# Kernel tuning notes

Measured on AMD Instinct MI355X. Metric: run time of the kernel, lower is better.

## Reference

```python
import jax, jax.numpy as jnp
import numpy as np


def _ln(x, g, b, eps=1e-5):
    m = jnp.mean(x, axis=-1, keepdims=True)
    v = jnp.var(x, axis=-1, keepdims=True)
    return (x - m) * jax.lax.rsqrt(v + eps) * g + b


def setup_inputs() -> dict:
    key = jax.random.key(0)
    ks = jax.random.split(key, 24)
    B, Cin, Cout, Rout, N1, N2 = 8, 256, 512, 256, 4096, 1024
    s = 0.02
    f32 = jnp.float32
    return {
        "l1": jax.random.normal(ks[0], (B, Cin, N1), f32),
        "xyz1": jax.random.normal(ks[1], (B, 3, N1), f32),
        "l2": jax.random.normal(ks[2], (B, Cout, N2), f32),
        "xyz2": jax.random.normal(ks[3], (B, 3, N2), f32),
        # im_choose 1x1 convs (no bias)
        "q1_w": jax.random.normal(ks[4], (Cout, Cin), f32) * s,
        "k1_w": jax.random.normal(ks[5], (Cout, Cin), f32) * s,
        # mlp: Linear(Cin,Cin) -> LN(Cin) -> ReLU -> Linear(Cin,Cout)
        "mlp_w1": jax.random.normal(ks[6], (Cin, Cin), f32) * s,
        "mlp_b1": jnp.zeros((Cin,), f32),
        "mlp_g1": jnp.ones((Cin,), f32),
        "mlp_be1": jnp.zeros((Cin,), f32),
        "mlp_w2": jax.random.normal(ks[7], (Cout, Cin), f32) * s,
        "mlp_b2": jnp.zeros((Cout,), f32),
        # slefAttention 1x1 convs (no bias); pos1 conv is unused in forward
        "qw": jax.random.normal(ks[8], (Cout, Cout), f32) * s,
        "kw": jax.random.normal(ks[9], (Cout, Cout), f32) * s,
        "vw": jax.random.normal(ks[10], (Cout, Cout), f32) * s,
        "posw": jax.random.normal(ks[11], (Cout, 3), f32) * s,
        # IMFF.norm LayerNorm(Cout)
        "norm_g": jnp.ones((Cout,), f32),
        "norm_b": jnp.zeros((Cout,), f32),
        # mlp1: Linear(Cout,Cout) -> LN(Cout) -> ReLU -> Linear(Cout,Rout)
        "m1_w1": jax.random.normal(ks[12], (Cout, Cout), f32) * s,
        "m1_b1": jnp.zeros((Cout,), f32),
        "m1_g": jnp.ones((Cout,), f32),
        "m1_be": jnp.zeros((Cout,), f32),
        "m1_w2": jax.random.normal(ks[13], (Rout, Cout), f32) * s,
        "m1_b2": jnp.zeros((Rout,), f32),
    }


def reference(l1, xyz1, l2, xyz2, q1_w, k1_w, mlp_w1, mlp_b1, mlp_g1, mlp_be1,
              mlp_w2, mlp_b2, qw, kw, vw, posw, norm_g, norm_b,
              m1_w1, m1_b1, m1_g, m1_be, m1_w2, m1_b2):
    Cout = q1_w.shape[0]
    top_k = l2.shape[2]
    scale = jnp.sqrt(jnp.float32(Cout))

    # ---- im_choose: top-k selection of source points via attention row 0 ----
    q1 = jnp.einsum('oc,bcn->bon', q1_w, l1)          # [B,Cout,N1]
    k1 = jnp.einsum('oc,bcn->bon', k1_w, l1)          # [B,Cout,N1]
    e1 = jnp.einsum('bcn,bcm->bnm', q1, k1) / scale   # [B,N1,N1]
    att1 = jax.nn.softmax(e1, axis=-1)
    att_se = att1[:, 0, :]                            # [B,N1]
    _, idx = jax.lax.top_k(att_se, top_k)             # [B,K]
    l1_sel = jnp.take_along_axis(l1, idx[:, None, :], axis=-1)    # [B,Cin,K]
    p1_sel = jnp.take_along_axis(xyz1, idx[:, None, :], axis=-1)  # [B,3,K]

    # ---- mlp on gathered features ----
    h = jnp.swapaxes(l1_sel, 1, 2)                    # [B,K,Cin]
    h = jax.nn.relu(_ln(h @ mlp_w1.T + mlp_b1, mlp_g1, mlp_be1))
    h = h @ mlp_w2.T + mlp_b2                         # [B,K,Cout]
    x2 = jnp.swapaxes(h, 1, 2)                        # [B,Cout,K]

    # ---- slefAttention (cross): x1=l2/xyz2 queries, x2/p1_sel keys+values ----
    pos_q = jnp.einsum('oc,bcn->bon', posw, xyz2)     # [B,Cout,N2]
    pos_k = jnp.einsum('oc,bcn->bon', posw, p1_sel)   # [B,Cout,K]
    q = jnp.einsum('oc,bcn->bon', qw, l2 + pos_q)
    k = jnp.einsum('oc,bcn->bon', kw, x2 + pos_k)
    v = jnp.einsum('oc,bcn->bon', vw, x2)
    e = jnp.einsum('bcn,bcm->bnm', q, k) / scale      # [B,N2,K]
    att = jax.nn.softmax(e, axis=-1)
    o = jnp.einsum('bnm,bcm->bcn', att, v) + l2       # [B,Cout,N2]
    o = jnp.swapaxes(o, 1, 2)                         # [B,N2,Cout]

    # ---- norm + leaky_relu + mlp1 head ----
    o = jax.nn.leaky_relu(_ln(o, norm_g, norm_b), 0.01)
    o = jax.nn.relu(_ln(o @ m1_w1.T + m1_b1, m1_g, m1_be))
    o = o @ m1_w2.T + m1_b2                           # [B,N2,Rout]
    return jnp.swapaxes(o, 1, 2)                      # [B,Rout,N2]
```

## Files before the change

### kernel.cpp

```cpp
#include <hip/hip_runtime.h>
#include <math.h>


typedef __attribute__((ext_vector_type(8))) short short8x;
typedef __attribute__((ext_vector_type(4))) float f32x4;

__device__ __forceinline__ unsigned short f2b(float f) {
  unsigned int u = __float_as_uint(f);
  unsigned int r = u + 0x7FFFu + ((u >> 16) & 1u);
  return (unsigned short)(r >> 16);
}
__device__ __forceinline__ float b2f(unsigned short h) {
  return __uint_as_float(((unsigned int)h) << 16);
}

__device__ __forceinline__ void cp16(const unsigned short* g, unsigned short* l) {
  __builtin_amdgcn_global_load_lds(
      (const __attribute__((address_space(1))) void*)g,
      (__attribute__((address_space(3))) void*)l, 16, 0, 0);
}

__global__ void __launch_bounds__(256) prep_kernel(
    const float* w0, const float* w1, const float* w2, const float* w3,
    const float* w4, const float* w5, const float* w6,
    unsigned short* d0, unsigned short* d1, unsigned short* d2,
    unsigned short* d3, unsigned short* d4, unsigned short* d5,
    unsigned short* d6,
    const float* __restrict__ l1, const float* __restrict__ q1w,
    float* __restrict__ q1v,
    const float* __restrict__ l2, const float* __restrict__ xyz2,
    const float* __restrict__ posw, unsigned short* __restrict__ qinT,
    float* __restrict__ l2T) {
  __shared__ float tile[64][65];
  __shared__ float sx[3][64];
  __shared__ float col[256];
  const int t = threadIdx.x;
  const int y = blockIdx.y;

  if (y == 7) {
    if (blockIdx.x >= 1024) return;
    const int b = blockIdx.x >> 7;
    const int rem = blockIdx.x & 127;
    const int n0 = (rem & 15) * 64, c0 = (rem >> 4) * 64;
    const int tx = t & 63, ty = t >> 6;
    const float* l2b = l2 + (long)b * 512 * 1024;
    for (int r = 0; r < 16; ++r) {
      const int c = ty * 16 + r;
      tile[c][tx] = l2b[(long)(c0 + c) * 1024 + n0 + tx];
    }
    if (ty < 3) sx[ty][tx] = xyz2[((long)b * 3 + ty) * 1024 + n0 + tx];
    __syncthreads();
    const int c = c0 + tx;
    const float p0 = posw[c * 3], p1 = posw[c * 3 + 1], p2 = posw[c * 3 + 2];
    for (int r = 0; r < 16; ++r) {
      const int nl = ty * 16 + r;
      const float val = tile[tx][nl];
      const long o = ((long)b * 1024 + n0 + nl) * 512 + c;
      l2T[o] = val;
      qinT[o] = f2b(val + p0 * sx[0][nl] + p1 * sx[1][nl] + p2 * sx[2][nl]);
    }
    return;
  }
  if (y == 8) {
    if (blockIdx.x >= 64) return;
    const int b = blockIdx.x >> 3;
    const int chunk = blockIdx.x & 7;
    col[t] = l1[(long)b * 256 * 4096 + (long)t * 4096];
    __syncthreads();
    const int lane = t & 63, wid = t >> 6;
    const float4 cv = *(const float4*)&col[lane * 4];
    const int obase = chunk * 64 + wid * 16;
#pragma unroll
    for (int oo = 0; oo < 16; ++oo) {
      const int o = obase + oo;
      const float4 wv = ((const float4*)(q1w + (long)o * 256))[lane];
      float s = wv.x * cv.x + wv.y * cv.y + wv.z * cv.z + wv.w * cv.w;
      s += __shfl_xor(s, 1); s += __shfl_xor(s, 2); s += __shfl_xor(s, 4);
      s += __shfl_xor(s, 8); s += __shfl_xor(s, 16); s += __shfl_xor(s, 32);
      if (lane == 0) q1v[b * 512 + o] = s;
    }
    return;
  }
  const float* src;
  unsigned short* dst;
  int n;
  switch (y) {
    case 0: src = w0; dst = d0; n = 65536; break;
    case 1: src = w1; dst = d1; n = 131072; break;
    case 2: src = w2; dst = d2; n = 262144; break;
    case 3: src = w3; dst = d3; n = 262144; break;
    case 4: src = w4; dst = d4; n = 262144; break;
    case 5: src = w5; dst = d5; n = 262144; break;
    default: src = w6; dst = d6; n = 131072; break;
  }
  const int i = (blockIdx.x * 256 + t) * 4;
  if (i < n) {
    const float4 v = *(const float4*)(src + i);
    ushort4 o;
    o.x = f2b(v.x); o.y = f2b(v.y); o.z = f2b(v.z); o.w = f2b(v.w);
    *(ushort4*)(dst + i) = o;
  }
}

__global__ void __launch_bounds__(256) selB_kernel(
    const float* __restrict__ k1w, const float* __restrict__ q1v,
    float* __restrict__ wvec) {
  const int b = blockIdx.x;
  const int chunk = blockIdx.y;
  __shared__ float qs[64];
  const int t = threadIdx.x;
  if (t < 64) qs[t] = q1v[b * 512 + chunk * 64 + t];
  __syncthreads();
  float s = 0.f;
  const float* kp = k1w + (long)(chunk * 64) * 256 + t;
#pragma unroll 8
  for (int oo = 0; oo < 64; ++oo) s += kp[(long)oo * 256] * qs[oo];
  atomicAdd(&wvec[b * 256 + t], s);
}

__global__ void __launch_bounds__(256) sel_scores_kernel(
    const float* __restrict__ l1, const float* __restrict__ wvec,
    float* __restrict__ scores) {
  const int b = blockIdx.y;
  const int m = blockIdx.x * 256 + threadIdx.x;
  __shared__ float w[256];
  w[threadIdx.x] = wvec[b * 256 + threadIdx.x];
  __syncthreads();
  const float* base = l1 + (long)b * 256 * 4096 + m;
  float s = 0.f;
  for (int c = 0; c < 256; ++c) s += w[c] * base[(long)c * 4096];
  scores[b * 4096 + m] = s;
}

__global__ void __launch_bounds__(256) topk_select_kernel(
    const float* __restrict__ scores, int* __restrict__ idx_out) {
  const int b = blockIdx.x;
  const int t = threadIdx.x;
  __shared__ unsigned int keys[4096];
  __shared__ unsigned int hist[256];
  __shared__ unsigned int sc_prefix, sc_krem;
  __shared__ int s_bin;
  __shared__ unsigned int partial_gt[256], partial_eq[256];

  for (int m = t; m < 4096; m += 256) {
    unsigned int u = __float_as_uint(scores[b * 4096 + m]);
    u ^= (u & 0x80000000u) ? 0xFFFFFFFFu : 0x80000000u;
    keys[m] = u;
  }
  if (t == 0) { sc_prefix = 0u; sc_krem = 1024u; }
  __syncthreads();

  unsigned int prefmask = 0u;
  for (int shift = 24; shift >= 0; shift -= 8) {
    hist[t] = 0u;
    if (t == 0) s_bin = 0;
    __syncthreads();
    const unsigned int prefix = sc_prefix;
    for (int m = t; m < 4096; m += 256) {
      unsigned int key = keys[m];
      if ((key & prefmask) == prefix) atomicAdd(&hist[(key >> shift) & 255u], 1u);
    }
    __syncthreads();
    for (int off = 1; off < 256; off <<= 1) {
      unsigned int v = hist[t] + ((t + off < 256) ? hist[t + off] : 0u);
      __syncthreads();
      hist[t] = v;
      __syncthreads();
    }
    const unsigned int krem = sc_krem;
    if (hist[t] >= krem) atomicMax(&s_bin, t);
    __syncthreads();
    if (t == 0) {
      const int bin = s_bin;
      sc_krem = krem - ((bin < 255) ? hist[bin + 1] : 0u);
      sc_prefix = prefix | ((unsigned int)bin << shift);
    }
    prefmask |= (0xFFu << shift);
    __syncthreads();
  }
  const unsigned int cutoff = sc_prefix;
  const unsigned int need = sc_krem;

  unsigned int gt = 0u, eq = 0u;
  const int base = t * 16;
  for (int i = 0; i < 16; ++i) {
    unsigned int key = keys[base + i];
    gt += (key > cutoff);
    eq += (key == cutoff);
  }
  partial_gt[t] = gt;
  partial_eq[t] = eq;
  __syncthreads();
  for (int off = 1; off < 256; off <<= 1) {
    unsigned int g = partial_gt[t] + ((t >= off) ? partial_gt[t - off] : 0u);
    unsigned int e2 = partial_eq[t] + ((t >= off) ? partial_eq[t - off] : 0u);
    __syncthreads();
    partial_gt[t] = g;
    partial_eq[t] = e2;
    __syncthreads();
  }
  const unsigned int pref_gt = partial_gt[t] - gt;
  const unsigned int pref_eq = partial_eq[t] - eq;
  unsigned int pos = pref_gt + ((pref_eq < need) ? pref_eq : need);
  unsigned int eqr = pref_eq;
  for (int i = 0; i < 16; ++i) {
    unsigned int key = keys[base + i];
    bool sel = (key > cutoff);
    if (key == cutoff) sel = sel || (eqr++ < need);
    if (sel) idx_out[b * 1024 + (pos++)] = base + i;
  }
}

__global__ void __launch_bounds__(256) gather_sel_kernel(
    const float* __restrict__ l1, const float* __restrict__ xyz1,
    const int* __restrict__ idx, unsigned short* __restrict__ l1selT,
    float* __restrict__ p1selT) {
  const int b = blockIdx.z;
  const int j = blockIdx.x * 64 + (threadIdx.x & 63);
  const int cz = blockIdx.y;
  const int cg = threadIdx.x >> 6;
  const int ix = idx[b * 1024 + j];
  const float* src = l1 + (long)b * 256 * 4096 + ix;
  unsigned short* dst = l1selT + ((long)b * 1024 + j) * 256;
#pragma unroll
  for (int it = 0; it < 8; ++it) {
    const int c = cz * 128 + it * 16 + cg * 4;
    const float x0 = src[(long)(c + 0) * 4096];
    const float x1 = src[(long)(c + 1) * 4096];
    const float x2 = src[(long)(c + 2) * 4096];
    const float x3 = src[(long)(c + 3) * 4096];
    ushort4 o;
    o.x = f2b(x0); o.y = f2b(x1); o.z = f2b(x2); o.w = f2b(x3);
    *(ushort4*)&dst[c] = o;
  }
  if (cz == 0 && cg == 0) {
    float* dp = p1selT + ((long)b * 1024 + j) * 3;
#pragma unroll
    for (int d = 0; d < 3; ++d) dp[d] = xyz1[((long)b * 3 + d) * 4096 + ix];
  }
}

template <int BN, int TRA, int TRB, bool BCOL, bool BROW, bool RES, int EPI>
__global__ void __launch_bounds__(256) gemm_u(
    const unsigned short* __restrict__ A, long sA, int ldA,
    const unsigned short* __restrict__ Bt, long sB, int ldB, long sB8,
    void* __restrict__ Yv, long sY, int ldY,
    const float* __restrict__ bias,
    const float* __restrict__ res, long sR,
    int K, float alpha,
    const float* __restrict__ ts1, const float* __restrict__ ts2,
    const float* __restrict__ tg, const float* __restrict__ tb, float tslope,
    float* __restrict__ os1, float* __restrict__ os2,
    const float* __restrict__ kpos, const float* __restrict__ kpw,
    unsigned short* __restrict__ Y2) {
  constexpr int JN = BN / 32;
  __shared__ __align__(16) unsigned short ldsA[2][128 * 32];
  __shared__ __align__(16) unsigned short ldsB[2][BN * 32];
  const int tid = threadIdx.x;
  const int lane = tid & 63;
  const int wv = tid >> 6;
  const int wm = wv >> 1, wn = wv & 1;
  const int n0 = blockIdx.x * BN, m0 = blockIdx.y * 128, b = blockIdx.z;
  A += (long)b * sA;
  Bt += (long)(b & 7) * sB + (long)(b >> 3) * sB8;
  const int lane15 = lane & 15, q = lane >> 4;

  const int srow0 = wv * 32 + (lane >> 2);
  const int srow1 = srow0 + 16;
  const int ks0 = ((lane & 3) ^ ((srow0 >> 1) & 3)) << 3;
  const int ks1 = ((lane & 3) ^ ((srow1 >> 1) & 3)) << 3;
  const unsigned short* gA0 = A + (long)(m0 + srow0) * ldA + ks0;
  const unsigned short* gA1 = A + (long)(m0 + srow1) * ldA + ks1;
  unsigned short* lA0[2] = {&ldsA[0][(wv * 32) * 32], &ldsA[1][(wv * 32) * 32]};
  unsigned short* lA1[2] = {&ldsA[0][(wv * 32 + 16) * 32], &ldsA[1][(wv * 32 + 16) * 32]};
  const int srowB = (BN == 128) ? srow0 : (wv * 16 + (lane >> 2));
  const int ksB = ((lane & 3) ^ ((srowB >> 1) & 3)) << 3;
  const unsigned short* gB0 = Bt + (long)(n0 + srowB) * ldB + ksB;
  const unsigned short* gB1 = Bt + (long)(n0 + srow1) * ldB + ks1;
  unsigned short* lB0[2] = {&ldsB[0][((BN == 128 ? wv * 32 : wv * 16)) * 32],
                            &ldsB[1][((BN == 128 ? wv * 32 : wv * 16)) * 32]};
  unsigned short* lB1[2] = {&ldsB[0][((wv * 32 + 16) * 32) % (BN * 32)],
                            &ldsB[1][((wv * 32 + 16) * 32) % (BN * 32)]};

  constexpr bool TR = (TRA + TRB) != 0;
  constexpr int TROWS = TRA ? 128 : BN;
  constexpr int TSH = (TROWS == 128) ? 7 : 6;
  constexpr int TCH = (TROWS == 128) ? 2 : 1;
  const int trow = tid & (TROWS - 1), tpart = tid >> TSH;
  float t_mu = 0.f, t_rs = 0.f;
  const unsigned short* tsrc = nullptr;
  int toff[2] = {0, 0};
  int tkof = 0;
  if constexpr (TR) {
    const int row0 = (TRA ? m0 : n0) + trow;
    const int ridx = (b & 7) * 1024 + row0;
    const float Cf = (float)K;
    const float s1v = ts1[ridx], s2v = ts2[ridx];
    t_mu = s1v / Cf;
    t_rs = rsqrtf(s2v / Cf - t_mu * t_mu + 1e-5f);
    tkof = tpart * (TCH * 8);
    tsrc = (TRA ? A + (long)row0 * ldA : Bt + (long)row0 * ldB) + tkof;
    const int sw = (trow >> 1) & 3;
#pragma unroll
    for (int c = 0; c < TCH; ++c)
      toff[c] = trow * 32 + (((tpart * TCH + c) ^ sw) << 3);
  }

  auto t_apply = [&](int kk, short8x r0, short8x r1, int buf) {
    unsigned short* base = TRA ? &ldsA[buf][0] : &ldsB[buf][0];
    const short8x rr[2] = {r0, r1};
#pragma unroll
    for (int c = 0; c < TCH; ++c) {
      union { short8x v; unsigned short u[8]; } a0, w0;
      a0.v = rr[c];
      const float4* gp = (const float4*)(tg + kk + tkof + c * 8);
      const float4* bp = (const float4*)(tb + kk + tkof + c * 8);
      const float4 g0 = gp[0], g1 = gp[1];
      const float4 e0 = bp[0], e1 = bp[1];
      const float gg[8] = {g0.x, g0.y, g0.z, g0.w, g1.x, g1.y, g1.z, g1.w};
      const float ee[8] = {e0.x, e0.y, e0.z, e0.w, e1.x, e1.y, e1.z, e1.w};
#pragma unroll
      for (int u = 0; u < 8; ++u) {
        float y = (b2f(a0.u[u]) - t_mu) * t_rs * gg[u] + ee[u];
        y = y > 0.f ? y : tslope * y;
        w0.u[u] = f2b(y);
      }
      *(short8x*)&base[toff[c]] = w0.v;
    }
  };

  short8x tr0 = {}, tr1 = {};
  if constexpr (TR) {
    tr0 = *(const short8x*)(tsrc + 0);
    if constexpr (TCH == 2) tr1 = *(const short8x*)(tsrc + 8);
  }
  if constexpr (!TRA) { cp16(gA0, lA0[0]); cp16(gA1, lA1[0]); }
  if constexpr (!TRB) {
    cp16(gB0, lB0[0]);
    if constexpr (BN == 128) cp16(gB1, lB1[0]);
  }
  if constexpr (TR) t_apply(0, tr0, tr1, 0);

  f32x4 acc[4][JN] = {};
  int cur = 0;
  for (int k0 = 0; k0 < K; k0 += 32) {
    __syncthreads();
    const bool nxt = (k0 + 32 < K);
    if (nxt) {
      const int nk = k0 + 32;
      if constexpr (!TRA) { cp16(gA0 + nk, lA0[cur ^ 1]); cp16(gA1 + nk, lA1[cur ^ 1]); }
      if constexpr (!TRB) {
        cp16(gB0 + nk, lB0[cur ^ 1]);
        if constexpr (BN == 128) cp16(gB1 + nk, lB1[cur ^ 1]);
      }
      if constexpr (TR) {
        tr0 = *(const short8x*)(tsrc + nk);
        if constexpr (TCH == 2) tr1 = *(const short8x*)(tsrc + nk + 8);
      }
    }
    short8x af[4], bfr[JN];
#pragma unroll
    for (int i = 0; i < 4; ++i) {
      const int m = wm * 64 + i * 16 + lane15;
      af[i] = *(const short8x*)&ldsA[cur][m * 32 + ((q ^ ((m >> 1) & 3)) << 3)];
    }
#pragma unroll
    for (int j = 0; j < JN; ++j) {
      const int n = wn * (BN / 2) + j * 16 + lane15;
      bfr[j] = *(const short8x*)&ldsB[cur][n * 32 + ((q ^ ((n >> 1) & 3)) << 3)];
    }
#pragma unroll
    for (int i = 0; i < 4; ++i)
#pragma unroll
      for (int j = 0; j < JN; ++j)
        acc[i][j] = __builtin_amdgcn_mfma_f32_16x16x32_bf16(af[i], bfr[j], acc[i][j], 0, 0, 0);
    if (nxt) {
      if constexpr (TR) t_apply(k0 + 32, tr0, tr1, cur ^ 1);
    }
    cur ^= 1;
  }

  float* Yf = (float*)Yv;
  unsigned short* Yh = (unsigned short*)Yv;
  if constexpr (EPI == 0) Yf += (long)b * sY; else Yh += (long)b * sY;
  if constexpr (EPI == 5) Y2 += (long)b * sY;
  if constexpr (RES) res += (long)b * sR;
  float inv_[4];
  float kq0[4], kq1[4], kq2[4];
  float ssum[4][4], ssq[4][4];
#pragma unroll
  for (int i = 0; i < 4; ++i)
#pragma unroll
    for (int r = 0; r < 4; ++r) { ssum[i][r] = 0.f; ssq[i][r] = 0.f; }

#pragma unroll
  for (int i = 0; i < 4; ++i) {
    if constexpr (EPI == 4) {
#pragma unroll
      for (int r = 0; r < 4; ++r)
        inv_[r] = 1.f / ts1[(b & 7) * 1024 + m0 + wm * 64 + i * 16 + q * 4 + r];
    }
    if constexpr (EPI == 5) {
#pragma unroll
      for (int r = 0; r < 4; ++r) {
        const int m_g = m0 + wm * 64 + i * 16 + q * 4 + r;
        const float* pp = kpos + ((long)b * 1024 + m_g) * 3;
        kq0[r] = pp[0]; kq1[r] = pp[1]; kq2[r] = pp[2];
      }
    }
#pragma unroll
    for (int j = 0; j < JN; ++j) {
      const int n_g = n0 + wn * (BN / 2) + j * 16 + lane15;
      const float bc = BCOL ? bias[n_g] : 0.f;
      float pw0 = 0.f, pw1 = 0.f, pw2 = 0.f;
      if constexpr (EPI == 5) {
        pw0 = kpw[n_g * 3]; pw1 = kpw[n_g * 3 + 1]; pw2 = kpw[n_g * 3 + 2];
      }
#pragma unroll
      for (int r = 0; r < 4; ++r) {
        const int m_g = m0 + wm * 64 + i * 16 + q * 4 + r;
        float y = acc[i][j][r] * alpha;
        if constexpr (EPI == 4) y *= inv_[r];
        if constexpr (BCOL) y += bc;
        if constexpr (BROW) y += bias[m_g];
        if constexpr (RES) y += res[(long)m_g * ldY + n_g];
        if constexpr (EPI == 3) y = __expf(y);
        const long off = (long)m_g * ldY + n_g;
        if constexpr (EPI == 0) Yf[off] = y;
        else Yh[off] = f2b(y);
        if constexpr (EPI == 5)
          Y2[off] = f2b(y + pw0 * kq0[r] + pw1 * kq1[r] + pw2 * kq2[r]);
        if constexpr (EPI == 2 || EPI == 3 || EPI == 4) {
          ssum[i][r] += y; ssq[i][r] += y * y;
        }
      }
    }
  }
  if constexpr (EPI == 2 || EPI == 4) {
#pragma unroll
    for (int i = 0; i < 4; ++i)
#pragma unroll
      for (int r = 0; r < 4; ++r) {
        float s = ssum[i][r], q2 = ssq[i][r];
        s += __shfl_xor(s, 1); q2 += __shfl_xor(q2, 1);
        s += __shfl_xor(s, 2); q2 += __shfl_xor(q2, 2);
        s += __shfl_xor(s, 4); q2 += __shfl_xor(q2, 4);
        s += __shfl_xor(s, 8); q2 += __shfl_xor(q2, 8);
        if (lane15 == 0) {
          const int ridx = (b & 7) * 1024 + m0 + wm * 64 + i * 16 + q * 4 + r;
          atomicAdd(&os1[ridx], s);
          atomicAdd(&os2[ridx], q2);
        }
      }
  } else if constexpr (EPI == 3) {
#pragma unroll
    for (int i = 0; i < 4; ++i)
#pragma unroll
      for (int r = 0; r < 4; ++r) {
        float s = ssum[i][r];
        s += __shfl_xor(s, 1);
        s += __shfl_xor(s, 2);
        s += __shfl_xor(s, 4);
        s += __shfl_xor(s, 8);
        if (lane15 == 0) {
          const int ridx = (b & 7) * 1024 + m0 + wm * 64 + i * 16 + q * 4 + r;
          atomicAdd(&os1[ridx], s);
        }
      }
  }
}

extern "C" void kernel_launch(void* const* d_in, const int* in_sizes, int n_in,
                              void* d_out, int out_size, void* d_ws,
                              size_t ws_size, hipStream_t stream) {
  const float* l1 = (const float*)d_in[0];
  const float* xyz1 = (const float*)d_in[1];
  const float* l2 = (const float*)d_in[2];
  const float* xyz2 = (const float*)d_in[3];
  const float* q1w = (const float*)d_in[4];
  const float* k1w = (const float*)d_in[5];
  const float* mlp_w1 = (const float*)d_in[6];
  const float* mlp_b1 = (const float*)d_in[7];
  const float* mlp_g1 = (const float*)d_in[8];
  const float* mlp_be1 = (const float*)d_in[9];
  const float* mlp_w2 = (const float*)d_in[10];
  const float* mlp_b2 = (const float*)d_in[11];
  const float* qw = (const float*)d_in[12];
  const float* kw = (const float*)d_in[13];
  const float* vw = (const float*)d_in[14];
  const float* posw = (const float*)d_in[15];
  const float* norm_g = (const float*)d_in[16];
  const float* norm_b = (const float*)d_in[17];
  const float* m1_w1 = (const float*)d_in[18];
  const float* m1_b1 = (const float*)d_in[19];
  const float* m1_g = (const float*)d_in[20];
  const float* m1_be = (const float*)d_in[21];
  const float* m1_w2 = (const float*)d_in[22];
  const float* m1_b2 = (const float*)d_in[23];

  char* ws = (char*)d_ws;
  const long MiB = 1048576;
  unsigned short* wb_mlp_w1 = (unsigned short*)(ws + 0);
  unsigned short* wb_mlp_w2 = (unsigned short*)(ws + 131072);
  unsigned short* wb_qw = (unsigned short*)(ws + 393216);
  unsigned short* wb_kw = (unsigned short*)(ws + 917504);
  unsigned short* wb_vw = (unsigned short*)(ws + 1441792);
  unsigned short* wb_m1w1 = (unsigned short*)(ws + 1966080);
  unsigned short* wb_m1w2 = (unsigned short*)(ws + 2490368);
  float* scores = (float*)(ws + 2752512);
  int* idxb = (int*)(ws + 2891776);
  float* p1selT = (float*)(ws + 2924544);
  float* q1v = (float*)(ws + 3022848);
  float* wvec = (float*)(ws + 3399680);
  float* rowsum = (float*)(ws + 3407872);
  float* h1_s1 = (float*)(ws + 3440640);
  float* h1_s2 = (float*)(ws + 3473408);
  float* o_s1 = (float*)(ws + 3506176);
  float* o_s2 = (float*)(ws + 3538944);
  float* g1_s1 = (float*)(ws + 3571712);
  float* g1_s2 = (float*)(ws + 3604480);
  unsigned short* l1selT = (unsigned short*)(ws + 4 * MiB);
  unsigned short* h1 = (unsigned short*)(ws + 8 * MiB);
  unsigned short* x2T = (unsigned short*)(ws + 12 * MiB);
  unsigned short* qinT = (unsigned short*)(ws + 20 * MiB);
  unsigned short* kinT = (unsigned short*)(ws + 28 * MiB);
  float* l2T = (float*)(ws + 36 * MiB);
  unsigned short* qT = (unsigned short*)(ws + 52 * MiB);
  unsigned short* kT = (unsigned short*)(ws + 60 * MiB);
  unsigned short* vbf = (unsigned short*)(ws + 68 * MiB);
  unsigned short* pbuf = (unsigned short*)(ws + 76 * MiB);
  unsigned short* obuf = (unsigned short*)(ws + 92 * MiB);
  unsigned short* g1buf = (unsigned short*)(ws + 100 * MiB);
  float* outp = (float*)d_out;

  const float inv_scale = 1.0f / sqrtf(512.0f);
  const long T256 = 1024L * 256, T512 = 1024L * 512, T1024 = 1024L * 1024;

  hipMemsetAsync(ws + 3399680, 0, 237568, stream);

  prep_kernel<<<dim3(1024, 9), 256, 0, stream>>>(
      mlp_w1, mlp_w2, qw, kw, vw, m1_w1, m1_w2,
      wb_mlp_w1, wb_mlp_w2, wb_qw, wb_kw, wb_vw, wb_m1w1, wb_m1w2,
      l1, q1w, q1v, l2, xyz2, posw, qinT, l2T);
  selB_kernel<<<dim3(8, 8), 256, 0, stream>>>(k1w, q1v, wvec);
  sel_scores_kernel<<<dim3(16, 8), 256, 0, stream>>>(l1, wvec, scores);
  topk_select_kernel<<<8, 256, 0, stream>>>(scores, idxb);
  gather_sel_kernel<<<dim3(16, 2, 8), 256, 0, stream>>>(l1, xyz1, idxb, l1selT, p1selT);

  gemm_u<64, 0, 0, true, false, false, 2><<<dim3(4, 8, 8), 256, 0, stream>>>(
      l1selT, T256, 256, wb_mlp_w1, 0, 256, 0, h1, T256, 256, mlp_b1,
      nullptr, 0, 256, 1.0f, nullptr, nullptr, nullptr, nullptr, 0.f,
      h1_s1, h1_s2, nullptr, nullptr, nullptr);
  gemm_u<64, 1, 0, true, false, false, 5><<<dim3(8, 8, 8), 256, 0, stream>>>(
      h1, T256, 256, wb_mlp_w2, 0, 256, 0, x2T, T512, 512, mlp_b2,
      nullptr, 0, 256, 1.0f, h1_s1, h1_s2, mlp_g1, mlp_be1, 0.f,
      nullptr, nullptr, p1selT, posw, kinT);

  gemm_u<64, 0, 0, false, false, false, 1><<<dim3(8, 8, 16), 256, 0, stream>>>(
      qinT, T512, 512, wb_qw, 0, 512, 262144, qT, T512, 512, nullptr,
      nullptr, 0, 512, 1.0f, nullptr, nullptr, nullptr, nullptr, 0.f,
      nullptr, nullptr, nullptr, nullptr, nullptr);
  gemm_u<64, 0, 0, false, false, false, 1><<<dim3(16, 4, 8), 256, 0, stream>>>(
      wb_vw, 0, 512, x2T, T512, 512, 0, vbf, T512, 1024, nullptr,
      nullptr, 0, 512, 1.0f, nullptr, nullptr, nullptr, nullptr, 0.f,
      nullptr, nullptr, nullptr, nullptr, nullptr);

  gemm_u<64, 0, 0, false, false, false, 3><<<dim3(16, 8, 8), 256, 0, stream>>>(
      qT, T512, 512, kT, T512, 512, 0, pbuf, T1024, 1024, nullptr,
      nullptr, 0, 512, inv_scale, nullptr, nullptr, nullptr, nullptr, 0.f,
      rowsum, nullptr, nullptr, nullptr, nullptr);
  gemm_u<64, 0, 0, false, false, true, 4><<<dim3(8, 8, 8), 256, 0, stream>>>(
      pbuf, T1024, 1024, vbf, T512, 1024, 0, obuf, T512, 512, nullptr,
      l2T, T512, 1024, 1.0f, rowsum, nullptr, nullptr, nullptr, 0.f,
      o_s1, o_s2, nullptr, nullptr, nullptr);
  gemm_u<64, 1, 0, true, false, false, 2><<<dim3(8, 8, 8), 256, 0, stream>>>(
      obuf, T512, 512, wb_m1w1, 0, 512, 0, g1buf, T512, 512, m1_b1,
      nullptr, 0, 512, 1.0f, o_s1, o_s2, norm_g, norm_b, 0.01f,
      g1_s1, g1_s2, nullptr, nullptr, nullptr);
  gemm_u<64, 0, 1, false, true, false, 0><<<dim3(16, 2, 8), 256, 0, stream>>>(
      wb_m1w2, 0, 512, g1buf, T512, 512, 0, outp, 256L * 1024, 1024, m1_b2,
      nullptr, 0, 512, 1.0f, g1_s1, g1_s2, m1_g, m1_be, 0.f,
      nullptr, nullptr, nullptr, nullptr, nullptr);
}
```

Before: 349.1 us.

## Fuse GEMM chain into persistent mega-kernel with grid-wide atomic barriers

Replaces eight separate GEMM launches with one persistent kernel of 512 blocks. The blocks loop over tiles of each stage and synchronise between stages through an atomic-counter grid barrier, and the q and v projections now share one stage. The aim is to remove launch gaps and tail effects between small dependent GEMMs. In exchange, every stage pays a spin-wait barrier, and the code relies on all 512 blocks being co-resident (launch bounds of 256 threads, 2 blocks per CU), otherwise it deadlocks.

```diff
diff --git a/kernel.cpp b/kernel.cpp
--- a/kernel.cpp
+++ b/kernel.cpp
@@ -18,6 +18,18 @@
   __builtin_amdgcn_global_load_lds(
       (const __attribute__((address_space(1))) void*)g,
       (__attribute__((address_space(3))) void*)l, 16, 0, 0);
+}
+
+__device__ __forceinline__ void gbar(int* bar, int target) {
+  __syncthreads();
+  __threadfence();
+  if (threadIdx.x == 0) {
+    __hip_atomic_fetch_add(bar, 1, __ATOMIC_ACQ_REL, __HIP_MEMORY_SCOPE_AGENT);
+    while (__hip_atomic_load(bar, __ATOMIC_ACQUIRE, __HIP_MEMORY_SCOPE_AGENT) < target)
+      __builtin_amdgcn_s_sleep(2);
+  }
+  __syncthreads();
+  __threadfence();
 }
 
 __global__ void __launch_bounds__(256) prep_kernel(
@@ -240,29 +252,31 @@
   }
 }
 
-template <int BN, int TRA, int TRB, bool BCOL, bool BROW, bool RES, int EPI>
-__global__ void __launch_bounds__(256) gemm_u(
-    const unsigned short* __restrict__ A, long sA, int ldA,
-    const unsigned short* __restrict__ Bt, long sB, int ldB, long sB8,
-    void* __restrict__ Yv, long sY, int ldY,
-    const float* __restrict__ bias,
-    const float* __restrict__ res, long sR,
-    int K, float alpha,
-    const float* __restrict__ ts1, const float* __restrict__ ts2,
-    const float* __restrict__ tg, const float* __restrict__ tb, float tslope,
-    float* __restrict__ os1, float* __restrict__ os2,
-    const float* __restrict__ kpos, const float* __restrict__ kpw,
-    unsigned short* __restrict__ Y2) {
-  constexpr int JN = BN / 32;
-  __shared__ __align__(16) unsigned short ldsA[2][128 * 32];
-  __shared__ __align__(16) unsigned short ldsB[2][BN * 32];
+struct GP {
+  const unsigned short* A; long sA; int ldA;
+  const unsigned short* Bt; long sB; int ldB; long sB8;
+  void* Yv; long sY; int ldY;
+  const float* bias; const float* res; long sR;
+  int K; float alpha;
+  const float* ts1; const float* ts2;
+  const float* tg; const float* tb; float tslope;
+  float* os1; float* os2;
+  const float* kpos; const float* kpw; unsigned short* Y2;
+};
+
+template <int TRA, int TRB, bool BCOL, bool BROW, bool RES, int EPI>
+__device__ void gemm_tile(const GP& p, int bx, int by, int bz,
+                          unsigned short* ldsA, unsigned short* ldsB) {
+  constexpr int BN = 64, JN = 2;
+  constexpr int ASTR = 128 * 32, BSTR = BN * 32;
   const int tid = threadIdx.x;
   const int lane = tid & 63;
   const int wv = tid >> 6;
   const int wm = wv >> 1, wn = wv & 1;
-  const int n0 = blockIdx.x * BN, m0 = blockIdx.y * 128, b = blockIdx.z;
-  A += (long)b * sA;
-  Bt += (long)(b & 7) * sB + (long)(b >> 3) * sB8;
+  const int n0 = bx * BN, m0 = by * 128, b = bz;
+  const unsigned short* A = p.A + (long)b * p.sA;
+  const unsigned short* Bt = p.Bt + (long)(b & 7) * p.sB + (long)(b >> 3) * p.sB8;
+  const int ldA = p.ldA, ldB = p.ldB, K = p.K;
   const int lane15 = lane & 15, q = lane >> 4;
 
   const int srow0 = wv * 32 + (lane >> 2);
@@ -271,16 +285,12 @@
   const int ks1 = ((lane & 3) ^ ((srow1 >> 1) & 3)) << 3;
   const unsigned short* gA0 = A + (long)(m0 + srow0) * ldA + ks0;
   const unsigned short* gA1 = A + (long)(m0 + srow1) * ldA + ks1;
-  unsigned short* lA0[2] = {&ldsA[0][(wv * 32) * 32], &ldsA[1][(wv * 32) * 32]};
-  unsigned short* lA1[2] = {&ldsA[0][(wv * 32 + 16) * 32], &ldsA[1][(wv * 32 + 16) * 32]};
-  const int srowB = (BN == 128) ? srow0 : (wv * 16 + (lane >> 2));
+  unsigned short* lA0[2] = {ldsA + (wv * 32) * 32, ldsA + ASTR + (wv * 32) * 32};
+  unsigned short* lA1[2] = {ldsA + (wv * 32 + 16) * 32, ldsA + ASTR + (wv * 32 + 16) * 32};
+  const int srowB = wv * 16 + (lane >> 2);
   const int ksB = ((lane & 3) ^ ((srowB >> 1) & 3)) << 3;
   const unsigned short* gB0 = Bt + (long)(n0 + srowB) * ldB + ksB;
-  const unsigned short* gB1 = Bt + (long)(n0 + srow1) * ldB + ks1;
-  unsigned short* lB0[2] = {&ldsB[0][((BN == 128 ? wv * 32 : wv * 16)) * 32],
-                            &ldsB[1][((BN == 128 ? wv * 32 : wv * 16)) * 32]};
-  unsigned short* lB1[2] = {&ldsB[0][((wv * 32 + 16) * 32) % (BN * 32)],
-                            &ldsB[1][((wv * 32 + 16) * 32) % (BN * 32)]};
+  unsigned short* lB0[2] = {ldsB + (wv * 16) * 32, ldsB + BSTR + (wv * 16) * 32};
 
   constexpr bool TR = (TRA + TRB) != 0;
   constexpr int TROWS = TRA ? 128 : BN;
@@ -295,7 +305,7 @@
     const int row0 = (TRA ? m0 : n0) + trow;
     const int ridx = (b & 7) * 1024 + row0;
     const float Cf = (float)K;
-    const float s1v = ts1[ridx], s2v = ts2[ridx];
+    const float s1v = p.ts1[ridx], s2v = p.ts2[ridx];
     t_mu = s1v / Cf;
     t_rs = rsqrtf(s2v / Cf - t_mu * t_mu + 1e-5f);
     tkof = tpart * (TCH * 8);
@@ -307,14 +317,14 @@
   }
 
   auto t_apply = [&](int kk, short8x r0, short8x r1, int buf) {
-    unsigned short* base = TRA ? &ldsA[buf][0] : &ldsB[buf][0];
+    unsigned short* base = TRA ? (ldsA + buf * ASTR) : (ldsB + buf * BSTR);
     const short8x rr[2] = {r0, r1};
 #pragma unroll
     for (int c = 0; c < TCH; ++c) {
       union { short8x v; unsigned short u[8]; } a0, w0;
       a0.v = rr[c];
-      const float4* gp = (const float4*)(tg + kk + tkof + c * 8);
-      const float4* bp = (const float4*)(tb + kk + tkof + c * 8);
+      const float4* gp = (const float4*)(p.tg + kk + tkof + c * 8);
+      const float4* bp = (const float4*)(p.tb + kk + tkof + c * 8);
       const float4 g0 = gp[0], g1 = gp[1];
       const float4 e0 = bp[0], e1 = bp[1];
       const float gg[8] = {g0.x, g0.y, g0.z, g0.w, g1.x, g1.y, g1.z, g1.w};
@@ -322,7 +332,7 @@
 #pragma unroll
       for (int u = 0; u < 8; ++u) {
         float y = (b2f(a0.u[u]) - t_mu) * t_rs * gg[u] + ee[u];
-        y = y > 0.f ? y : tslope * y;
+        y = y > 0.f ? y : p.tslope * y;
         w0.u[u] = f2b(y);
       }
       *(short8x*)&base[toff[c]] = w0.v;
@@ -335,10 +345,7 @@
     if constexpr (TCH == 2) tr1 = *(const short8x*)(tsrc + 8);
   }
   if constexpr (!TRA) { cp16(gA0, lA0[0]); cp16(gA1, lA1[0]); }
-  if constexpr (!TRB) {
-    cp16(gB0, lB0[0]);
-    if constexpr (BN == 128) cp16(gB1, lB1[0]);
-  }
+  if constexpr (!TRB) { cp16(gB0, lB0[0]); }
   if constexpr (TR) t_apply(0, tr0, tr1, 0);
 
   f32x4 acc[4][JN] = {};
@@ -349,10 +356,7 @@
     if (nxt) {
       const int nk = k0 + 32;
       if constexpr (!TRA) { cp16(gA0 + nk, lA0[cur ^ 1]); cp16(gA1 + nk, lA1[cur ^ 1]); }
-      if constexpr (!TRB) {
-        cp16(gB0 + nk, lB0[cur ^ 1]);
-        if constexpr (BN == 128) cp16(gB1 + nk, lB1[cur ^ 1]);
-      }
+      if constexpr (!TRB) { cp16(gB0 + nk, lB0[cur ^ 1]); }
       if constexpr (TR) {
         tr0 = *(const short8x*)(tsrc + nk);
         if constexpr (TCH == 2) tr1 = *(const short8x*)(tsrc + nk + 8);
@@ -362,12 +366,12 @@
 #pragma unroll
     for (int i = 0; i < 4; ++i) {
       const int m = wm * 64 + i * 16 + lane15;
-      af[i] = *(const short8x*)&ldsA[cur][m * 32 + ((q ^ ((m >> 1) & 3)) << 3)];
+      af[i] = *(const short8x*)&ldsA[cur * ASTR + m * 32 + ((q ^ ((m >> 1) & 3)) << 3)];
     }
 #pragma unroll
     for (int j = 0; j < JN; ++j) {
       const int n = wn * (BN / 2) + j * 16 + lane15;
-      bfr[j] = *(const short8x*)&ldsB[cur][n * 32 + ((q ^ ((n >> 1) & 3)) << 3)];
+      bfr[j] = *(const short8x*)&ldsB[cur * BSTR + n * 32 + ((q ^ ((n >> 1) & 3)) << 3)];
     }
 #pragma unroll
     for (int i = 0; i < 4; ++i)
@@ -380,11 +384,14 @@
     cur ^= 1;
   }
 
-  float* Yf = (float*)Yv;
-  unsigned short* Yh = (unsigned short*)Yv;
-  if constexpr (EPI == 0) Yf += (long)b * sY; else Yh += (long)b * sY;
-  if constexpr (EPI == 5) Y2 += (long)b * sY;
-  if constexpr (RES) res += (long)b * sR;
+  float* Yf = (float*)p.Yv;
+  unsigned short* Yh = (unsigned short*)p.Yv;
+  if constexpr (EPI == 0) Yf += (long)b * p.sY; else Yh += (long)b * p.sY;
+  unsigned short* Y2 = p.Y2;
+  if constexpr (EPI == 5) Y2 += (long)b * p.sY;
+  const float* res = p.res;
+  if constexpr (RES) res += (long)b * p.sR;
+  const int ldY = p.ldY;
   float inv_[4];
   float kq0[4], kq1[4], kq2[4];
   float ssum[4][4], ssq[4][4];
@@ -398,31 +405,31 @@
     if constexpr (EPI == 4) {
 #pragma unroll
       for (int r = 0; r < 4; ++r)
-        inv_[r] = 1.f / ts1[(b & 7) * 1024 + m0 + wm * 64 + i * 16 + q * 4 + r];
+        inv_[r] = 1.f / p.ts1[(b & 7) * 1024 + m0 + wm * 64 + i * 16 + q * 4 + r];
     }
     if constexpr (EPI == 5) {
 #pragma unroll
       for (int r = 0; r < 4; ++r) {
         const int m_g = m0 + wm * 64 + i * 16 + q * 4 + r;
-        const float* pp = kpos + ((long)b * 1024 + m_g) * 3;
+        const float* pp = p.kpos + ((long)b * 1024 + m_g) * 3;
         kq0[r] = pp[0]; kq1[r] = pp[1]; kq2[r] = pp[2];
       }
     }
 #pragma unroll
     for (int j = 0; j < JN; ++j) {
       const int n_g = n0 + wn * (BN / 2) + j * 16 + lane15;
-      const float bc = BCOL ? bias[n_g] : 0.f;
+      const float bc = BCOL ? p.bias[n_g] : 0.f;
       float pw0 = 0.f, pw1 = 0.f, pw2 = 0.f;
       if constexpr (EPI == 5) {
-        pw0 = kpw[n_g * 3]; pw1 = kpw[n_g * 3 + 1]; pw2 = kpw[n_g * 3 + 2];
+        pw0 = p.kpw[n_g * 3]; pw1 = p.kpw[n_g * 3 + 1]; pw2 = p.kpw[n_g * 3 + 2];
       }
 #pragma unroll
       for (int r = 0; r < 4; ++r) {
         const int m_g = m0 + wm * 64 + i * 16 + q * 4 + r;
-        float y = acc[i][j][r] * alpha;
+        float y = acc[i][j][r] * p.alpha;
         if constexpr (EPI == 4) y *= inv_[r];
         if constexpr (BCOL) y += bc;
-        if constexpr (BROW) y += bias[m_g];
+        if constexpr (BROW) y += p.bias[m_g];
         if constexpr (RES) y += res[(long)m_g * ldY + n_g];
         if constexpr (EPI == 3) y = __expf(y);
         const long off = (long)m_g * ldY + n_g;
@@ -448,8 +455,8 @@
         s += __shfl_xor(s, 8); q2 += __shfl_xor(q2, 8);
         if (lane15 == 0) {
           const int ridx = (b & 7) * 1024 + m0 + wm * 64 + i * 16 + q * 4 + r;
-          atomicAdd(&os1[ridx], s);
-          atomicAdd(&os2[ridx], q2);
+          atomicAdd(&p.os1[ridx], s);
+          atomicAdd(&p.os2[ridx], q2);
         }
       }
   } else if constexpr (EPI == 3) {
@@ -464,9 +471,147 @@
         s += __shfl_xor(s, 8);
         if (lane15 == 0) {
           const int ridx = (b & 7) * 1024 + m0 + wm * 64 + i * 16 + q * 4 + r;
-          atomicAdd(&os1[ridx], s);
+          atomicAdd(&p.os1[ridx], s);
         }
       }
+  }
+}
+
+__global__ void __launch_bounds__(256, 2) mega_kernel(
+    char* ws, float* outp,
+    const float* mlp_b1, const float* mlp_g1, const float* mlp_be1,
+    const float* mlp_b2, const float* posw,
+    const float* norm_g, const float* norm_b,
+    const float* m1_b1, const float* m1_g, const float* m1_be,
+    const float* m1_b2) {
+  __shared__ __align__(16) unsigned short sA[2 * 128 * 32];
+  __shared__ __align__(16) unsigned short sB[2 * 64 * 32];
+  const long MiB = 1048576;
+  unsigned short* wb_mlp_w1 = (unsigned short*)(ws + 0);
+  unsigned short* wb_mlp_w2 = (unsigned short*)(ws + 131072);
+  unsigned short* wb_qw = (unsigned short*)(ws + 393216);
+  unsigned short* wb_vw = (unsigned short*)(ws + 1441792);
+  unsigned short* wb_m1w1 = (unsigned short*)(ws + 1966080);
+  unsigned short* wb_m1w2 = (unsigned short*)(ws + 2490368);
+  float* p1selT = (float*)(ws + 2924544);
+  float* rowsum = (float*)(ws + 3407872);
+  float* h1_s1 = (float*)(ws + 3440640);
+  float* h1_s2 = (float*)(ws + 3473408);
+  float* o_s1 = (float*)(ws + 3506176);
+  float* o_s2 = (float*)(ws + 3538944);
+  float* g1_s1 = (float*)(ws + 3571712);
+  float* g1_s2 = (float*)(ws + 3604480);
+  int* bar = (int*)(ws + 3637248);
+  unsigned short* l1selT = (unsigned short*)(ws + 4 * MiB);
+  unsigned short* h1 = (unsigned short*)(ws + 8 * MiB);
+  unsigned short* x2T = (unsigned short*)(ws + 12 * MiB);
+  unsigned short* qinT = (unsigned short*)(ws + 20 * MiB);
+  unsigned short* kinT = (unsigned short*)(ws + 28 * MiB);
+  float* l2T = (float*)(ws + 36 * MiB);
+  unsigned short* qT = (unsigned short*)(ws + 52 * MiB);
+  unsigned short* kT = (unsigned short*)(ws + 60 * MiB);
+  unsigned short* vbf = (unsigned short*)(ws + 68 * MiB);
+  unsigned short* pbuf = (unsigned short*)(ws + 76 * MiB);
+  unsigned short* obuf = (unsigned short*)(ws + 92 * MiB);
+  unsigned short* g1buf = (unsigned short*)(ws + 100 * MiB);
+
+  const long T256 = 1024L * 256, T512 = 1024L * 512, T1024 = 1024L * 1024;
+  const float inv_scale = 0.04419417382415922f;
+  const int NB = gridDim.x;
+
+  {
+    GP p{.A = l1selT, .sA = T256, .ldA = 256, .Bt = wb_mlp_w1, .sB = 0,
+         .ldB = 256, .sB8 = 0, .Yv = h1, .sY = T256, .ldY = 256,
+         .bias = mlp_b1, .res = nullptr, .sR = 0, .K = 256, .alpha = 1.0f,
+         .ts1 = nullptr, .ts2 = nullptr, .tg = nullptr, .tb = nullptr,
+         .tslope = 0.f, .os1 = h1_s1, .os2 = h1_s2, .kpos = nullptr,
+         .kpw = nullptr, .Y2 = nullptr};
+    for (int t = blockIdx.x; t < 256; t += NB)
+      gemm_tile<0, 0, true, false, false, 2>(p, t & 3, (t >> 2) & 7, t >> 5, sA, sB);
+  }
+  gbar(bar, NB * 1);
+
+  {
+    GP p{.A = h1, .sA = T256, .ldA = 256, .Bt = wb_mlp_w2, .sB = 0,
+         .ldB = 256, .sB8 = 0, .Yv = x2T, .sY = T512, .ldY = 512,
+         .bias = mlp_b2, .res = nullptr, .sR = 0, .K = 256, .alpha = 1.0f,
+         .ts1 = h1_s1, .ts2 = h1_s2, .tg = mlp_g1, .tb = mlp_be1,
+         .tslope = 0.f, .os1 = nullptr, .os2 = nullptr, .kpos = p1selT,
+         .kpw = posw, .Y2 = kinT};
+    for (int t = blockIdx.x; t < 512; t += NB)
+      gemm_tile<1, 0, true, false, false, 5>(p, t & 7, (t >> 3) & 7, t >> 6, sA, sB);
+  }
+  gbar(bar, NB * 2);
+
+  {
+    GP pq{.A = qinT, .sA = T512, .ldA = 512, .Bt = wb_qw, .sB = 0,
+          .ldB = 512, .sB8 = 262144, .Yv = qT, .sY = T512, .ldY = 512,
+          .bias = nullptr, .res = nullptr, .sR = 0, .K = 512, .alpha = 1.0f,
+          .ts1 = nullptr, .ts2 = nullptr, .tg = nullptr, .tb = nullptr,
+          .tslope = 0.f, .os1 = nullptr, .os2 = nullptr, .kpos = nullptr,
+          .kpw = nullptr, .Y2 = nullptr};
+    GP pv{.A = wb_vw, .sA = 0, .ldA = 512, .Bt = x2T, .sB = T512,
+          .ldB = 512, .sB8 = 0, .Yv = vbf, .sY = T512, .ldY = 1024,
+          .bias = nullptr, .res = nullptr, .sR = 0, .K = 512, .alpha = 1.0f,
+          .ts1 = nullptr, .ts2 = nullptr, .tg = nullptr, .tb = nullptr,
+          .tslope = 0.f, .os1 = nullptr, .os2 = nullptr, .kpos = nullptr,
+          .kpw = nullptr, .Y2 = nullptr};
+    for (int t = blockIdx.x; t < 1536; t += NB) {
+      if (t < 1024) {
+        gemm_tile<0, 0, false, false, false, 1>(pq, t & 7, (t >> 3) & 7, t >> 6, sA, sB);
+      } else {
+        const int u = t - 1024;
+        gemm_tile<0, 0, false, false, false, 1>(pv, u & 15, (u >> 4) & 3, u >> 6, sA, sB);
+      }
+    }
+  }
+  gbar(bar, NB * 3);
+
+  {
+    GP p{.A = qT, .sA = T512, .ldA = 512, .Bt = kT, .sB = T512,
+         .ldB = 512, .sB8 = 0, .Yv = pbuf, .sY = T1024, .ldY = 1024,
+         .bias = nullptr, .res = nullptr, .sR = 0, .K = 512,
+         .alpha = inv_scale, .ts1 = nullptr, .ts2 = nullptr, .tg = nullptr,
+         .tb = nullptr, .tslope = 0.f, .os1 = rowsum, .os2 = nullptr,
+         .kpos = nullptr, .kpw = nullptr, .Y2 = nullptr};
+    for (int t = blockIdx.x; t < 1024; t += NB)
+      gemm_tile<0, 0, false, false, false, 3>(p, t & 15, (t >> 4) & 7, t >> 7, sA, sB);
+  }
+  gbar(bar, NB * 4);
+
+  {
+    GP p{.A = pbuf, .sA = T1024, .ldA = 1024, .Bt = vbf, .sB = T512,
+         .ldB = 1024, .sB8 = 0, .Yv = obuf, .sY = T512, .ldY = 512,
+         .bias = nullptr, .res = l2T, .sR = T512, .K = 1024, .alpha = 1.0f,
+         .ts1 = rowsum, .ts2 = nullptr, .tg = nullptr, .tb = nullptr,
+         .tslope = 0.f, .os1 = o_s1, .os2 = o_s2, .kpos = nullptr,
+         .kpw = nullptr, .Y2 = nullptr};
+    for (int t = blockIdx.x; t < 512; t += NB)
+      gemm_tile<0, 0, false, false, true, 4>(p, t & 7, (t >> 3) & 7, t >> 6, sA, sB);
+  }
+  gbar(bar, NB * 5);
+
+  {
+    GP p{.A = obuf, .sA = T512, .ldA = 512, .Bt = wb_m1w1, .sB = 0,
+         .ldB = 512, .sB8 = 0, .Yv = g1buf, .sY = T512, .ldY = 512,
+         .bias = m1_b1, .res = nullptr, .sR = 0, .K = 512, .alpha = 1.0f,
+         .ts1 = o_s1, .ts2 = o_s2, .tg = norm_g, .tb = norm_b,
+         .tslope = 0.01f, .os1 = g1_s1, .os2 = g1_s2, .kpos = nullptr,
+         .kpw = nullptr, .Y2 = nullptr};
+    for (int t = blockIdx.x; t < 512; t += NB)
+      gemm_tile<1, 0, true, false, false, 2>(p, t & 7, (t >> 3) & 7, t >> 6, sA, sB);
+  }
+  gbar(bar, NB * 6);
+
+  {
+    GP p{.A = wb_m1w2, .sA = 0, .ldA = 512, .Bt = g1buf, .sB = T512,
+         .ldB = 512, .sB8 = 0, .Yv = outp, .sY = 256L * 1024, .ldY = 1024,
+         .bias = m1_b2, .res = nullptr, .sR = 0, .K = 512, .alpha = 1.0f,
+         .ts1 = g1_s1, .ts2 = g1_s2, .tg = m1_g, .tb = m1_be,
+         .tslope = 0.f, .os1 = nullptr, .os2 = nullptr, .kpos = nullptr,
+         .kpw = nullptr, .Y2 = nullptr};
+    for (int t = blockIdx.x; t < 256; t += NB)
+      gemm_tile<0, 1, false, true, false, 0>(p, t & 15, (t >> 4) & 1, t >> 5, sA, sB);
   }
 }
 
@@ -499,7 +644,6 @@
   const float* m1_b2 = (const float*)d_in[23];
 
   char* ws = (char*)d_ws;
-  const long MiB = 1048576;
   unsigned short* wb_mlp_w1 = (unsigned short*)(ws + 0);
   unsigned short* wb_mlp_w2 = (unsigned short*)(ws + 131072);
   unsigned short* wb_qw = (unsigned short*)(ws + 393216);
@@ -512,31 +656,12 @@
   float* p1selT = (float*)(ws + 2924544);
   float* q1v = (float*)(ws + 3022848);
   float* wvec = (float*)(ws + 3399680);
-  float* rowsum = (float*)(ws + 3407872);
-  float* h1_s1 = (float*)(ws + 3440640);
-  float* h1_s2 = (float*)(ws + 3473408);
-  float* o_s1 = (float*)(ws + 3506176);
-  float* o_s2 = (float*)(ws + 3538944);
-  float* g1_s1 = (float*)(ws + 3571712);
-  float* g1_s2 = (float*)(ws + 3604480);
+  const long MiB = 1048576;
   unsigned short* l1selT = (unsigned short*)(ws + 4 * MiB);
-  unsigned short* h1 = (unsigned short*)(ws + 8 * MiB);
-  unsigned short* x2T = (unsigned short*)(ws + 12 * MiB);
   unsigned short* qinT = (unsigned short*)(ws + 20 * MiB);
-  unsigned short* kinT = (unsigned short*)(ws + 28 * MiB);
   float* l2T = (float*)(ws + 36 * MiB);
-  unsigned short* qT = (unsigned short*)(ws + 52 * MiB);
-  unsigned short* kT = (unsigned short*)(ws + 60 * MiB);
-  unsigned short* vbf = (unsigned short*)(ws + 68 * MiB);
-  unsigned short* pbuf = (unsigned short*)(ws + 76 * MiB);
-  unsigned short* obuf = (unsigned short*)(ws + 92 * MiB);
-  unsigned short* g1buf = (unsigned short*)(ws + 100 * MiB);
-  float* outp = (float*)d_out;
-
-  const float inv_scale = 1.0f / sqrtf(512.0f);
-  const long T256 = 1024L * 256, T512 = 1024L * 512, T1024 = 1024L * 1024;
-
-  hipMemsetAsync(ws + 3399680, 0, 237568, stream);
+
+  hipMemsetAsync(ws + 3399680, 0, 241664, stream);
 
   prep_kernel<<<dim3(1024, 9), 256, 0, stream>>>(
       mlp_w1, mlp_w2, qw, kw, vw, m1_w1, m1_w2,
@@ -547,38 +672,7 @@
   topk_select_kernel<<<8, 256, 0, stream>>>(scores, idxb);
   gather_sel_kernel<<<dim3(16, 2, 8), 256, 0, stream>>>(l1, xyz1, idxb, l1selT, p1selT);
 
-  gemm_u<64, 0, 0, true, false, false, 2><<<dim3(4, 8, 8), 256, 0, stream>>>(
-      l1selT, T256, 256, wb_mlp_w1, 0, 256, 0, h1, T256, 256, mlp_b1,
-      nullptr, 0, 256, 1.0f, nullptr, nullptr, nullptr, nullptr, 0.f,
-      h1_s1, h1_s2, nullptr, nullptr, nullptr);
-  gemm_u<64, 1, 0, true, false, false, 5><<<dim3(8, 8, 8), 256, 0, stream>>>(
-      h1, T256, 256, wb_mlp_w2, 0, 256, 0, x2T, T512, 512, mlp_b2,
-      nullptr, 0, 256, 1.0f, h1_s1, h1_s2, mlp_g1, mlp_be1, 0.f,
-      nullptr, nullptr, p1selT, posw, kinT);
-
-  gemm_u<64, 0, 0, false, false, false, 1><<<dim3(8, 8, 16), 256, 0, stream>>>(
-      qinT, T512, 512, wb_qw, 0, 512, 262144, qT, T512, 512, nullptr,
-      nullptr, 0, 512, 1.0f, nullptr, nullptr, nullptr, nullptr, 0.f,
-      nullptr, nullptr, nullptr, nullptr, nullptr);
-  gemm_u<64, 0, 0, false, false, false, 1><<<dim3(16, 4, 8), 256, 0, stream>>>(
-      wb_vw, 0, 512, x2T, T512, 512, 0, vbf, T512, 1024, nullptr,
-      nullptr, 0, 512, 1.0f, nullptr, nullptr, nullptr, nullptr, 0.f,
-      nullptr, nullptr, nullptr, nullptr, nullptr);
-
-  gemm_u<64, 0, 0, false, false, false, 3><<<dim3(16, 8, 8), 256, 0, stream>>>(
-      qT, T512, 512, kT, T512, 512, 0, pbuf, T1024, 1024, nullptr,
-      nullptr, 0, 512, inv_scale, nullptr, nullptr, nullptr, nullptr, 0.f,
-      rowsum, nullptr, nullptr, nullptr, nullptr);
-  gemm_u<64, 0, 0, false, false, true, 4><<<dim3(8, 8, 8), 256, 0, stream>>>(
-      pbuf, T1024, 1024, vbf, T512, 1024, 0, obuf, T512, 512, nullptr,
-      l2T, T512, 1024, 1.0f, rowsum, nullptr, nullptr, nullptr, 0.f,
-      o_s1, o_s2, nullptr, nullptr, nullptr);
-  gemm_u<64, 1, 0, true, false, false, 2><<<dim3(8, 8, 8), 256, 0, stream>>>(
-      obuf, T512, 512, wb_m1w1, 0, 512, 0, g1buf, T512, 512, m1_b1,
-      nullptr, 0, 512, 1.0f, o_s1, o_s2, norm_g, norm_b, 0.01f,
-      g1_s1, g1_s2, nullptr, nullptr, nullptr);
-  gemm_u<64, 0, 1, false, true, false, 0><<<dim3(16, 2, 8), 256, 0, stream>>>(
-      wb_m1w2, 0, 512, g1buf, T512, 512, 0, outp, 256L * 1024, 1024, m1_b2,
-      nullptr, 0, 512, 1.0f, g1_s1, g1_s2, m1_g, m1_be, 0.f,
-      nullptr, nullptr, nullptr, nullptr, nullptr);
-}
+  mega_kernel<<<512, 256, 0, stream>>>(
+      ws, (float*)d_out, mlp_b1, mlp_g1, mlp_be1, mlp_b2, posw,
+      norm_g, norm_b, m1_b1, m1_g, m1_be, m1_b2);
+}
```

Measured after the change: 1.049 ms. +200.6%, slower.
